# Performance work log

Measured on AMD Instinct MI355X. Metric: run time of the kernel, lower is better.

The kernel has to match this reference:

```python
import jax, jax.numpy as jnp
import numpy as np

B = 4096
HIST = 50
VOCAB = 100000
PAD_IDX = 179
EMB_DIM = 64           # sparse_dim_after_embedding
DENSE = 256            # dense_feature_number
PROJ_IN = 768          # emb_feature_dim_before_project
PROJ_HID = 256
PROJ_OUT = 64          # emb_feature_dim
BOT = (512, 64)        # bottom_mlp_dims
ALL_DIM = EMB_DIM + BOT[1] + PROJ_OUT        # 192
OUT_DIM = ALL_DIM * (ALL_DIM + 1) // 2 + BOT[1]  # 18592
TOP = (1024, 512)      # top_mlp_dims
BN_EPS = 1e-5

# precomputed upper-triangular (incl. diagonal) indices, row-major like torch mask extract
_TRIU_R, _TRIU_C = np.triu_indices(ALL_DIM)


def setup_inputs() -> dict:
    key = jax.random.key(0)
    ks = jax.random.split(key, 20)
    s = 0.02
    emb_table = jax.random.normal(ks[0], (VOCAB, EMB_DIM), jnp.float32) * s
    emb_table = emb_table.at[PAD_IDX].set(0.0)  # padding_idx=179
    return {
        "x_sparse": jax.random.randint(ks[1], (B, HIST), 0, VOCAB),
        "x_dense": jax.random.normal(ks[2], (B, DENSE), jnp.float32),
        "x_embed_before_projection": jax.random.normal(ks[3], (B, PROJ_IN), jnp.float32),
        "emb_table": emb_table,
        "pw1": jax.random.normal(ks[4], (PROJ_IN, PROJ_HID), jnp.float32) * s,
        "pb1": jnp.zeros((PROJ_HID,), jnp.float32),
        "pw2": jax.random.normal(ks[5], (PROJ_HID, PROJ_OUT), jnp.float32) * s,
        "pb2": jnp.zeros((PROJ_OUT,), jnp.float32),
        "bn_gamma": jnp.ones((PROJ_OUT,), jnp.float32),
        "bn_beta": jnp.zeros((PROJ_OUT,), jnp.float32),
        "bw1": jax.random.normal(ks[6], (DENSE, BOT[0]), jnp.float32) * s,
        "bb1": jnp.zeros((BOT[0],), jnp.float32),
        "bw2": jax.random.normal(ks[7], (BOT[0], BOT[1]), jnp.float32) * s,
        "bb2": jnp.zeros((BOT[1],), jnp.float32),
        "tw1": jax.random.normal(ks[8], (OUT_DIM, TOP[0]), jnp.float32) * s,
        "tb1": jnp.zeros((TOP[0],), jnp.float32),
        "tw2": jax.random.normal(ks[9], (TOP[0], TOP[1]), jnp.float32) * s,
        "tb2": jnp.zeros((TOP[1],), jnp.float32),
        "tw3": jax.random.normal(ks[10], (TOP[1], 1), jnp.float32) * s,
        "tb3": jnp.zeros((1,), jnp.float32),
    }


def reference(x_sparse, x_dense, x_embed_before_projection, emb_table,
              pw1, pb1, pw2, pb2, bn_gamma, bn_beta,
              bw1, bb1, bw2, bb2, tw1, tb1, tw2, tb2, tw3, tb3):
    # embedding-sum over history: [B, HIST, EMB_DIM] -> [B, EMB_DIM]
    embed_x = jnp.sum(emb_table[x_sparse], axis=1)

    # ContrastiveNet: Linear -> ReLU -> Linear -> BatchNorm1d (batch stats, training fwd)
    h = jax.nn.relu(x_embed_before_projection @ pw1 + pb1)
    z = h @ pw2 + pb2
    mu = jnp.mean(z, axis=0)
    var = jnp.var(z, axis=0)  # biased variance, as torch BN uses for normalization
    x_embed = bn_gamma * (z - mu) * jax.lax.rsqrt(var + BN_EPS) + bn_beta

    # bottom MLP (dropout = identity at inference)
    bottom = jax.nn.relu(jax.nn.relu(x_dense @ bw1 + bb1) @ bw2 + bb2)

    concat_first = jnp.concatenate([bottom, x_embed, embed_x], axis=-1)  # [B, 192]

    # pairwise dot-product interaction; pack upper triangle incl. diagonal
    dot = jnp.einsum('bi,bj->bij', concat_first, concat_first)  # [B, 192, 192]
    interaction = dot[:, _TRIU_R, _TRIU_C]  # [B, 192*193/2]

    concat_second = jnp.concatenate([interaction, bottom], axis=-1)  # [B, OUT_DIM]

    t = jax.nn.relu(concat_second @ tw1 + tb1)
    t = jax.nn.relu(t @ tw2 + tb2)
    output = jax.nn.sigmoid(t @ tw3 + tb3)  # [B, 1]
    # squeeze(-1).squeeze().unsqueeze(1) -> [B, 1]
    output = output.reshape(-1, 1)
    return output, x_embed
```

## Files before the change

kernel.cpp:

```cpp
#include <hip/hip_runtime.h>
#include <hip/hip_bf16.h>
#include <cstdint>
#include <cstddef>

typedef __bf16 bf16;
typedef unsigned char u8;
typedef __bf16 v8bf  __attribute__((ext_vector_type(8)));
typedef float  f32x4 __attribute__((ext_vector_type(4)));
typedef float  f32x16 __attribute__((ext_vector_type(16)));
typedef int    i32x4 __attribute__((ext_vector_type(4)));
typedef int    v8i32 __attribute__((ext_vector_type(8)));

__device__ __forceinline__ void async16(void* lds, const void* g) {
  __builtin_amdgcn_global_load_lds(
      (const __attribute__((address_space(1))) unsigned int*)g,
      (__attribute__((address_space(3))) unsigned int*)lds, 16, 0, 0);
}



__device__ __forceinline__ void pairs_dev(int* __restrict__ pairs) {
  int r = threadIdx.x;
  if (r < 192) {
    int off = 192 * r - (r * (r - 1)) / 2;
    for (int c = r; c < 192; ++c) pairs[off + c - r] = (r << 16) | c;
  } else if (r == 192) {
    for (int j = 0; j < 64; ++j) pairs[18528 + j] = (j << 16) | 192;
  } else if (r == 193) {
    for (int j = 18592; j < 18624; ++j) pairs[j] = (192 << 16) | 192;
  }
}

__device__ __forceinline__ void packA_dev(const float* __restrict__ A,
                                          bf16* __restrict__ Ap, int K,
                                          int bx, int by) {
  const int t = threadIdx.x;
  const int KT = K >> 5;
  const size_t tile = ((size_t)bx * KT + by) * (64 * 32);
  const int c = t;
  const int mm = c >> 2, koct = (c & 3) * 8;
  const float* src = A + (size_t)(bx * 64 + mm) * K + by * 32 + koct;
  f32x4 f0 = *(const f32x4*)src;
  f32x4 f1 = *(const f32x4*)(src + 4);
  __align__(16) bf16 h[8];
  h[0]=(bf16)f0[0]; h[1]=(bf16)f0[1]; h[2]=(bf16)f0[2]; h[3]=(bf16)f0[3];
  h[4]=(bf16)f1[0]; h[5]=(bf16)f1[1]; h[6]=(bf16)f1[2]; h[7]=(bf16)f1[3];
  *(i32x4*)(Ap + tile + (size_t)c * 8) = *(const i32x4*)h;
}

__device__ __forceinline__ void packB_dev(const float* __restrict__ B,
                                          bf16* __restrict__ Bp, int K, int N,
                                          int bx, int by,
                                          float* __restrict__ sLB) {
  const int BNp = 64, LS = 66;
  const int t = threadIdx.x;
  const int KT = K >> 5;
  for (int idx = t; idx < 32 * BNp; idx += 256) {
    const int kk = idx >> 6, nn = idx & 63;
    sLB[kk * LS + nn] = B[(size_t)(by * 32 + kk) * N + bx * BNp + nn];
  }
  __syncthreads();
  const size_t tile = ((size_t)bx * KT + by) * ((size_t)BNp * 32);
  for (int c = t; c < BNp * 4; c += 256) {
    const int nn = c >> 2, koct = (c & 3) * 8;
    __align__(16) bf16 h[8];
#pragma unroll
    for (int j = 0; j < 8; ++j) h[j] = (bf16)sLB[(koct + j) * LS + nn];
    *(i32x4*)(Bp + tile + (size_t)c * 8) = *(const i32x4*)h;
  }
}

__device__ __forceinline__ void packTw1_dev(const float* __restrict__ tw1,
                                            u8* __restrict__ Bp, int nt, int kw,
                                            float* __restrict__ sLB) {
  const int t = threadIdx.x;
  for (int idx = t; idx < 64 * 128; idx += 256) {
    const int kk = idx >> 7, nn = idx & 127;
    const int gk = kw * 64 + kk;
    sLB[kk * 130 + nn] = (gk < 18592) ? tw1[(size_t)gk * 1024 + nt * 128 + nn] * 32.f : 0.f;
  }
  __syncthreads();
  u8* tile = Bp + ((size_t)nt * 291 + kw) * 8192;
  for (int c = t; c < 512; c += 256) {
    const int nn = c >> 2, kb = (c & 3) * 16;
    i32x4 d;
#pragma unroll
    for (int g = 0; g < 4; ++g) {
      const float p0 = sLB[(kb + g * 4 + 0) * 130 + nn];
      const float p1 = sLB[(kb + g * 4 + 1) * 130 + nn];
      const float p2 = sLB[(kb + g * 4 + 2) * 130 + nn];
      const float p3 = sLB[(kb + g * 4 + 3) * 130 + nn];
      int r = __builtin_amdgcn_cvt_pk_fp8_f32(p0, p1, 0, false);
      r = __builtin_amdgcn_cvt_pk_fp8_f32(p2, p3, r, true);
      d[g] = r;
    }
    *(i32x4*)(tile + c * 16) = d;
  }
}

__device__ __forceinline__ void embed_dev(const int* __restrict__ xs,
                                          const float* __restrict__ emb,
                                          float* __restrict__ cf, int blk) {
  const int wid = threadIdx.x >> 6, lane = threadIdx.x & 63;
  const int b = blk * 4 + wid;
  const int* row = xs + (size_t)b * 50;
  float acc = 0.f;
  for (int h = 0; h < 50; ++h) {
    int idx = row[h];
    acc += emb[(size_t)idx * 64 + lane];
  }
  cf[(size_t)b * 193 + 128 + lane] = acc;
}

__global__ __launch_bounds__(256) void prologue_kernel(
    const float* __restrict__ xep, const float* __restrict__ xd,
    const float* __restrict__ pw1, const float* __restrict__ pw2,
    const float* __restrict__ bw1, const float* __restrict__ bw2,
    const float* __restrict__ tw1, const float* __restrict__ tw2,
    const int* __restrict__ xs, const float* __restrict__ emb,
    bf16* Xp, bf16* Xd, bf16* Bpw1, bf16* Bpw2, bf16* Bbw1, bf16* Bbw2,
    u8* Btw1, bf16* Btw2, float* cf, int* pairs) {
  __shared__ float sLB[64 * 130];
  int i = blockIdx.x;
  if (i < 2328) { packTw1_dev(tw1, Btw1, i & 7, i >> 3, sLB); return; }
  i -= 2328;
  if (i < 1536) { packA_dev(xep, Xp, 768, i & 63, i >> 6); return; }
  i -= 1536;
  if (i < 512)  { packA_dev(xd, Xd, 256, i & 63, i >> 6); return; }
  i -= 512;
  if (i < 96)   { packB_dev(pw1, Bpw1, 768, 256, i & 3, i >> 2, sLB); return; }
  i -= 96;
  if (i < 8)    { packB_dev(pw2, Bpw2, 256, 64, 0, i, sLB); return; }
  i -= 8;
  if (i < 64)   { packB_dev(bw1, Bbw1, 256, 512, i & 7, i >> 3, sLB); return; }
  i -= 64;
  if (i < 16)   { packB_dev(bw2, Bbw2, 512, 64, 0, i, sLB); return; }
  i -= 16;
  if (i < 256)  { packB_dev(tw2, Btw2, 1024, 512, i & 7, i >> 3, sLB); return; }
  i -= 256;
  if (i < 1024) { embed_dev(xs, emb, cf, i); return; }
  i -= 1024;
  if (i == 0) pairs_dev(pairs);
}

template <int BM, int BN, int MF, int NF>
__device__ __forceinline__ void gemm_body(
    const bf16* __restrict__ Ap, const bf16* __restrict__ Bp,
    const float* __restrict__ bias,
    float* __restrict__ outF, int ldF,
    bf16* __restrict__ outP, int ktN, int bmsh,
    int KT, int M0, int relu_flag, int bx, int by,
    bf16* sA, bf16* sB) {
  const int t = threadIdx.x;
  const int wid = t >> 6, lane = t & 63;
  const int wm = (wid >> 1) * (MF * 16);
  const int wn = (wid & 1) * (NF * 16);
  const int r16 = lane & 15, q = lane >> 4;

  f32x4 acc[MF][NF];
#pragma unroll
  for (int i = 0; i < MF; ++i)
#pragma unroll
    for (int j = 0; j < NF; ++j) acc[i][j] = f32x4{0.f, 0.f, 0.f, 0.f};

  const bf16* aBase = Ap + (size_t)bx * KT * (BM * 32);
  const bf16* bBase = Bp + (size_t)by * KT * (BN * 32);
  constexpr int A_CH = BM * 4;
  constexpr int B_CH = BN * 4;

  for (int kt = 0; kt < KT; ++kt) {
    const bf16* ag = aBase + (size_t)kt * (BM * 32);
    const bf16* bg = bBase + (size_t)kt * (BN * 32);
#pragma unroll
    for (int c = t; c < A_CH; c += 256) {
      const int row = c >> 2, qs = c & 3, qg = (qs - (row >> 1)) & 3;
      async16(sA + c * 8, ag + row * 32 + qg * 8);
    }
#pragma unroll
    for (int c = t; c < B_CH; c += 256) {
      const int row = c >> 2, qs = c & 3, qg = (qs - (row >> 1)) & 3;
      async16(sB + c * 8, bg + row * 32 + qg * 8);
    }
    __syncthreads();
    v8bf af[MF], bfr[NF];
#pragma unroll
    for (int i = 0; i < MF; ++i) {
      const int row = wm + i * 16 + r16;
      af[i] = *(const v8bf*)(sA + row * 32 + (((q + (row >> 1)) & 3) * 8));
    }
#pragma unroll
    for (int j = 0; j < NF; ++j) {
      const int row = wn + j * 16 + r16;
      bfr[j] = *(const v8bf*)(sB + row * 32 + (((q + (row >> 1)) & 3) * 8));
    }
#pragma unroll
    for (int i = 0; i < MF; ++i)
#pragma unroll
      for (int j = 0; j < NF; ++j)
        acc[i][j] = __builtin_amdgcn_mfma_f32_16x16x32_bf16(af[i], bfr[j], acc[i][j], 0, 0, 0);
    __syncthreads();
  }

#pragma unroll
  for (int j = 0; j < NF; ++j) {
    const int gn = by * BN + wn + j * 16 + r16;
    const float bv = bias[gn];
#pragma unroll
    for (int i = 0; i < MF; ++i) {
      const int gm0 = M0 + bx * BM + wm + i * 16 + q * 4;
#pragma unroll
      for (int r = 0; r < 4; ++r) {
        float v = acc[i][j][r] + bv;
        if (relu_flag) v = fmaxf(v, 0.f);
        const int gm = gm0 + r;
        if (outF) outF[(size_t)gm * ldF + gn] = v;
        if (outP) {
          const int mt = gm >> bmsh, mm = gm & ((1 << bmsh) - 1);
          outP[(((size_t)mt * ktN + (gn >> 5)) << (bmsh + 5)) + ((size_t)mm << 5) + (gn & 31)] = (bf16)v;
        }
      }
    }
  }
}

template <int BM, int BN, int MF, int NF>
__global__ __launch_bounds__(256, 2) void gemm_kernel(
    const bf16* __restrict__ Ap, const bf16* __restrict__ Bp,
    const float* __restrict__ bias,
    float* __restrict__ outF, int ldF,
    bf16* __restrict__ outP, int ktN, int bmsh,
    int KT, int M0, int relu_flag) {
  __shared__ __align__(16) bf16 sA[BM * 32];
  __shared__ __align__(16) bf16 sB[BN * 32];
  gemm_body<BM, BN, MF, NF>(Ap, Bp, bias, outF, ldF, outP, ktN, bmsh,
                            KT, M0, relu_flag, blockIdx.x, blockIdx.y, sA, sB);
}

template <int BM, int BN, int MF, int NF>
__global__ __launch_bounds__(256, 2) void gemm_dual_kernel(
    const bf16* Ap0, const bf16* Bp0, const float* bias0,
    float* outF0, int ldF0, bf16* outP0, int ktN0, int bmsh0, int KT0, int relu0, int gy0,
    const bf16* Ap1, const bf16* Bp1, const float* bias1,
    float* outF1, int ldF1, bf16* outP1, int ktN1, int bmsh1, int KT1, int relu1, int gy1) {
  __shared__ __align__(16) bf16 sA[BM * 32];
  __shared__ __align__(16) bf16 sB[BN * 32];
  if (blockIdx.z == 0) {
    if ((int)blockIdx.y >= gy0) return;
    gemm_body<BM, BN, MF, NF>(Ap0, Bp0, bias0, outF0, ldF0, outP0, ktN0, bmsh0,
                              KT0, 0, relu0, blockIdx.x, blockIdx.y, sA, sB);
  } else {
    if ((int)blockIdx.y >= gy1) return;
    gemm_body<BM, BN, MF, NF>(Ap1, Bp1, bias1, outF1, ldF1, outP1, ktN1, bmsh1,
                              KT1, 0, relu1, blockIdx.x, blockIdx.y, sA, sB);
  }
}

__global__ __launch_bounds__(256, 2) void gemm_splitk_mx(
    const u8* __restrict__ Ap, const u8* __restrict__ Bp,
    bf16* __restrict__ part, int S, int Mchunk) {
  __shared__ __align__(16) u8 sA[2][8192];
  __shared__ __align__(16) u8 sB[2][8192];
  const int t = threadIdx.x;
  const int bx = blockIdx.x, by = blockIdx.y, bz = blockIdx.z;
  const int wid = t >> 6, lane = t & 63;
  const int wm = (wid >> 1) * 64, wn = (wid & 1) * 64;
  const int l31 = lane & 31, khalf = lane >> 5;
  const int kw0 = (291 * bz) / S, kw1 = (291 * (bz + 1)) / S;

  f32x16 acc[2][2];
#pragma unroll
  for (int i = 0; i < 2; ++i)
#pragma unroll
    for (int j = 0; j < 2; ++j)
#pragma unroll
      for (int r = 0; r < 16; ++r) acc[i][j][r] = 0.f;

  const u8* aBase = Ap + (size_t)bx * 291 * 8192;
  const u8* bBase = Bp + (size_t)by * 291 * 8192;

  auto stage = [&](int buf, int kw) {
    const u8* ag = aBase + (size_t)kw * 8192;
    const u8* bg = bBase + (size_t)kw * 8192;
#pragma unroll
    for (int c = t; c < 512; c += 256) {
      const int row = c >> 2, qs = c & 3, qg = (qs - (row >> 1)) & 3;
      async16(sA[buf] + c * 16, ag + row * 64 + qg * 16);
    }
#pragma unroll
    for (int c = t; c < 512; c += 256) {
      const int row = c >> 2, qs = c & 3, qg = (qs - (row >> 1)) & 3;
      async16(sB[buf] + c * 16, bg + row * 64 + qg * 16);
    }
  };
  auto frag = [&](const u8* s, int row) -> v8i32 {
    const int q0 = (khalf * 2 + (row >> 1)) & 3;
    const int q1 = (khalf * 2 + 1 + (row >> 1)) & 3;
    union { i32x4 h[2]; v8i32 v; } u;
    u.h[0] = *(const i32x4*)(s + row * 64 + q0 * 16);
    u.h[1] = *(const i32x4*)(s + row * 64 + q1 * 16);
    return u.v;
  };
  auto compute = [&](int buf) {
    v8i32 av[2], bv[2];
#pragma unroll
    for (int i = 0; i < 2; ++i) av[i] = frag(sA[buf], wm + i * 32 + l31);
#pragma unroll
    for (int j = 0; j < 2; ++j) bv[j] = frag(sB[buf], wn + j * 32 + l31);
#pragma unroll
    for (int i = 0; i < 2; ++i)
#pragma unroll
      for (int j = 0; j < 2; ++j)
        acc[i][j] = __builtin_amdgcn_mfma_scale_f32_32x32x64_f8f6f4(
            av[i], bv[j], acc[i][j], 0, 0,
            0, 0x7F7F7F7F,
            0, 0x7A7A7A7A);
  };

  int kw = kw0;
  for (; kw + 1 < kw1; kw += 2) {
    stage(0, kw);
    stage(1, kw + 1);
    __syncthreads();
    compute(0);
    compute(1);
    __syncthreads();
  }
  if (kw < kw1) {
    stage(0, kw);
    __syncthreads();
    compute(0);
    __syncthreads();
  }

  bf16* pBase = part + (size_t)bz * Mchunk * 1024;
#pragma unroll
  for (int i = 0; i < 2; ++i)
#pragma unroll
    for (int j = 0; j < 2; ++j) {
      const int gn = by * 128 + wn + j * 32 + l31;
#pragma unroll
      for (int r = 0; r < 16; ++r) {
        const int gm = bx * 128 + wm + i * 32 + (r & 3) + 8 * (r >> 2) + 4 * khalf;
        pBase[(size_t)gm * 1024 + gn] = (bf16)acc[i][j][r];
      }
    }
}

__global__ __launch_bounds__(256) void reducek_kernel(const bf16* __restrict__ part,
                                                      const float* __restrict__ bias,
                                                      bf16* __restrict__ t1,
                                                      int S, int Mchunk, int M0) {
  const int idx = blockIdx.x * 256 + threadIdx.x;
  const int gm = idx >> 7;
  const int gn8 = (idx & 127) * 8;
  float v[8] = {0.f, 0.f, 0.f, 0.f, 0.f, 0.f, 0.f, 0.f};
  for (int s = 0; s < S; ++s) {
    v8bf p = *(const v8bf*)(part + ((size_t)s * Mchunk + gm) * 1024 + gn8);
#pragma unroll
    for (int r = 0; r < 8; ++r) v[r] += (float)p[r];
  }
  const f32x4 b0 = *(const f32x4*)(bias + gn8);
  const f32x4 b1 = *(const f32x4*)(bias + gn8 + 4);
  __align__(16) bf16 h[8];
#pragma unroll
  for (int r = 0; r < 4; ++r) h[r] = (bf16)fmaxf(v[r] + b0[r], 0.f);
#pragma unroll
  for (int r = 0; r < 4; ++r) h[4 + r] = (bf16)fmaxf(v[4 + r] + b1[r], 0.f);
  const int G = M0 + gm;
  const int mt = G >> 6, mm = G & 63, kt = gn8 >> 5;
  *(i32x4*)(t1 + (((size_t)mt * 32 + kt) << 11) + (mm << 5) + (gn8 & 31)) = *(const i32x4*)h;
}

__global__ __launch_bounds__(256) void bnstats_kernel(const float* __restrict__ z,
                                                      float* __restrict__ stats) {
  const int j = blockIdx.x, t = threadIdx.x;
  float s = 0.f, s2 = 0.f;
  for (int b = t; b < 4096; b += 256) {
    float v = z[(size_t)b * 64 + j];
    s += v; s2 += v * v;
  }
  __shared__ float sh[256], sh2[256];
  sh[t] = s; sh2[t] = s2;
  __syncthreads();
  for (int o = 128; o > 0; o >>= 1) {
    if (t < o) { sh[t] += sh[t + o]; sh2[t] += sh2[t + o]; }
    __syncthreads();
  }
  if (t == 0) {
    float mu = sh[0] * (1.f / 4096.f);
    float var = sh2[0] * (1.f / 4096.f) - mu * mu;
    stats[j] = mu;
    stats[64 + j] = rsqrtf(var + 1e-5f);
  }
}

__global__ __launch_bounds__(256) void cfbuild_kernel(const float* __restrict__ z,
                                                      const float* __restrict__ stats,
                                                      const float* __restrict__ gamma,
                                                      const float* __restrict__ beta,
                                                      float* __restrict__ cf,
                                                      float* __restrict__ dout) {
  const int wid = threadIdx.x >> 6, lane = threadIdx.x & 63;
  const int b = blockIdx.x * 4 + wid;
  const float mu = stats[lane], rstd = stats[64 + lane];
  const float xe = gamma[lane] * (z[(size_t)b * 64 + lane] - mu) * rstd + beta[lane];
  cf[(size_t)b * 193 + 64 + lane] = xe;
  dout[4096 + (size_t)b * 64 + lane] = xe;
  if (lane == 0) cf[(size_t)b * 193 + 192] = 1.f;
}

__global__ __launch_bounds__(256, 2) void agen_kernel(const float* __restrict__ cf,
                                                      const int* __restrict__ pairs,
                                                      u8* __restrict__ Ap, int rowBase) {
  __shared__ float sCF[64 * 193];
  const int t = threadIdx.x;
  const int gRow0 = rowBase + blockIdx.x * 64;
  for (int i = t; i < 64 * 193; i += 256) sCF[i] = cf[(size_t)gRow0 * 193 + i];
  __syncthreads();
  const int kw0 = (291 * blockIdx.y) / 8;
  const int kw1 = (291 * (blockIdx.y + 1)) / 8;
  const int row = t >> 2, kq = t & 3;
  const int mt = blockIdx.x >> 1;
  const int mrow = (blockIdx.x & 1) * 64 + row;
  const float* myrow = sCF + row * 193;
  for (int kw = kw0; kw < kw1; ++kw) {
    const int kb = kw * 64 + kq * 16;
    i32x4 d;
#pragma unroll
    for (int g = 0; g < 4; ++g) {
      float p[4];
#pragma unroll
      for (int j = 0; j < 4; ++j) {
        const int pr = pairs[kb + g * 4 + j];
        p[j] = myrow[pr >> 16] * myrow[pr & 0xffff];
      }
      int r = __builtin_amdgcn_cvt_pk_fp8_f32(p[0], p[1], 0, false);
      r = __builtin_amdgcn_cvt_pk_fp8_f32(p[2], p[3], r, true);
      d[g] = r;
    }
    *(i32x4*)(Ap + (((size_t)mt * 291 + kw) * 128 + mrow) * 64 + kq * 16) = d;
  }
}

__global__ __launch_bounds__(256) void topdot_kernel(const float* __restrict__ t2,
                                                     const float* __restrict__ w,
                                                     const float* __restrict__ b3,
                                                     float* __restrict__ dout) {
  const int wid = threadIdx.x >> 6, lane = threadIdx.x & 63;
  const int b = blockIdx.x * 4 + wid;
  const f32x4* row = (const f32x4*)(t2 + (size_t)b * 512);
  const f32x4* wv = (const f32x4*)w;
  float s = 0.f;
#pragma unroll
  for (int i = 0; i < 2; ++i) {
    f32x4 a = row[lane * 2 + i], c = wv[lane * 2 + i];
    s += a[0] * c[0] + a[1] * c[1] + a[2] * c[2] + a[3] * c[3];
  }
  for (int m = 32; m > 0; m >>= 1) s += __shfl_xor(s, m, 64);
  if (lane == 0) dout[b] = 1.f / (1.f + __expf(-(s + b3[0])));
}

extern "C" void kernel_launch(void* const* d_in, const int* in_sizes, int n_in,
                              void* d_out, int out_size, void* d_ws, size_t ws_size,
                              hipStream_t stream) {
  const int*   xs   = (const int*)  d_in[0];
  const float* xd   = (const float*)d_in[1];
  const float* xep  = (const float*)d_in[2];
  const float* emb  = (const float*)d_in[3];
  const float* pw1  = (const float*)d_in[4];
  const float* pb1  = (const float*)d_in[5];
  const float* pw2  = (const float*)d_in[6];
  const float* pb2  = (const float*)d_in[7];
  const float* gmma = (const float*)d_in[8];
  const float* beta = (const float*)d_in[9];
  const float* bw1  = (const float*)d_in[10];
  const float* bb1  = (const float*)d_in[11];
  const float* bw2  = (const float*)d_in[12];
  const float* bb2  = (const float*)d_in[13];
  const float* tw1  = (const float*)d_in[14];
  const float* tb1  = (const float*)d_in[15];
  const float* tw2  = (const float*)d_in[16];
  const float* tb2  = (const float*)d_in[17];
  const float* tw3  = (const float*)d_in[18];
  const float* tb3  = (const float*)d_in[19];
  float* out = (float*)d_out;

  uint8_t* base = (uint8_t*)d_ws;
  size_t off = 0;
  auto alloc = [&](size_t b) {
    void* p = base + off;
    off = (off + b + 511) & ~((size_t)511);
    return p;
  };
  int*  pairs = (int*) alloc((size_t)18624 * 4);
  bf16* Xp    = (bf16*)alloc((size_t)4096 * 768 * 2);
  bf16* Xd    = (bf16*)alloc((size_t)4096 * 256 * 2);
  bf16* Bpw1  = (bf16*)alloc((size_t)768 * 256 * 2);
  bf16* Bpw2  = (bf16*)alloc((size_t)256 * 64 * 2);
  bf16* Bbw1  = (bf16*)alloc((size_t)256 * 512 * 2);
  bf16* Bbw2  = (bf16*)alloc((size_t)512 * 64 * 2);
  u8*   Btw1  = (u8*)  alloc((size_t)8 * 291 * 8192);
  bf16* Btw2  = (bf16*)alloc((size_t)1024 * 512 * 2);
  bf16* hbuf  = (bf16*)alloc((size_t)4096 * 256 * 2);
  float* z    = (float*)alloc((size_t)4096 * 64 * 4);
  float* stats= (float*)alloc((size_t)128 * 4);
  bf16* b0    = (bf16*)alloc((size_t)4096 * 512 * 2);
  float* cf   = (float*)alloc((size_t)4096 * 193 * 4);
  bf16* t1    = (bf16*)alloc((size_t)4096 * 1024 * 2);
  float* t2   = (float*)alloc((size_t)4096 * 512 * 4);
  size_t fixedEnd = off;

  int chunk = 512, S = 8;
  {
    const int candC[5] = {4096, 4096, 2048, 1024, 512};
    const int candS[5] = {8, 4, 8, 8, 8};
    for (int i = 0; i < 5; ++i) {
      size_t need = fixedEnd + (size_t)candC[i] * 18624 + 1024 +
                    (size_t)candS[i] * candC[i] * 1024 * 2 + 1024;
      if (need <= ws_size) { chunk = candC[i]; S = candS[i]; break; }
    }
  }
  u8*   ApBig = (u8*)  alloc((size_t)chunk * 18624);
  bf16* partK = (bf16*)alloc((size_t)S * chunk * 1024 * 2);

  prologue_kernel<<<5841, 256, 0, stream>>>(
      xep, xd, pw1, pw2, bw1, bw2, tw1, tw2, xs, emb,
      Xp, Xd, Bpw1, Bpw2, Bbw1, Bbw2, Btw1, Btw2, cf, pairs);

  gemm_dual_kernel<64, 64, 2, 2><<<dim3(64, 8, 2), 256, 0, stream>>>(
      Xp, Bpw1, pb1, nullptr, 0, hbuf, 8, 6, 24, 1, 4,
      Xd, Bbw1, bb1, nullptr, 0, b0, 16, 6, 8, 1, 8);
  gemm_dual_kernel<64, 64, 2, 2><<<dim3(64, 1, 2), 256, 0, stream>>>(
      hbuf, Bpw2, pb2, z, 64, nullptr, 0, 0, 8, 0, 1,
      b0, Bbw2, bb2, cf, 193, nullptr, 0, 0, 16, 1, 1);

  bnstats_kernel<<<64, 256, 0, stream>>>(z, stats);
  cfbuild_kernel<<<1024, 256, 0, stream>>>(z, stats, gmma, beta, cf, out);

  for (int c0 = 0; c0 < 4096; c0 += chunk) {
    agen_kernel<<<dim3(chunk / 64, 8), 256, 0, stream>>>(cf, pairs, ApBig, c0);
    gemm_splitk_mx<<<dim3(chunk / 128, 8, S), 256, 0, stream>>>(
        ApBig, Btw1, partK, S, chunk);
    reducek_kernel<<<chunk / 2, 256, 0, stream>>>(partK, tb1, t1, S, chunk, c0);
  }

  gemm_kernel<64, 64, 2, 2><<<dim3(64, 8), 256, 0, stream>>>(
      t1, Btw2, tb2, t2, 512, nullptr, 0, 0, 32, 0, 1);
  topdot_kernel<<<1024, 256, 0, stream>>>(t2, tw3, tb3, out);
}
```

Before: 383.0 us.

## Vectorize tw1 packing, shrink pair table, move embedding into dual GEMM

Several changes land together. The tw1 fp8 packing now uses float4 loads into a smaller two-phase LDS tile (32x132). The pair index table is compressed to 16-bit entries that are loaded as vectors in agen. The embedding-bag sum moves out of the prologue into a third z-slice of the first dual GEMM launch, with 8 rows per block, so it overlaps with the GEMMs. The occupancy hint on the split-K fp8 GEMM is also raised to 3 blocks per SM, which may increase register pressure.

```diff
diff --git a/kernel.cpp b/kernel.cpp
--- a/kernel.cpp
+++ b/kernel.cpp
@@ -5,6 +5,7 @@
 
 typedef __bf16 bf16;
 typedef unsigned char u8;
+typedef unsigned short u16;
 typedef __bf16 v8bf  __attribute__((ext_vector_type(8)));
 typedef float  f32x4 __attribute__((ext_vector_type(4)));
 typedef float  f32x16 __attribute__((ext_vector_type(16)));
@@ -19,15 +20,15 @@
 
 
 
-__device__ __forceinline__ void pairs_dev(int* __restrict__ pairs) {
+__device__ __forceinline__ void pairs_dev(u16* __restrict__ pairs) {
   int r = threadIdx.x;
   if (r < 192) {
     int off = 192 * r - (r * (r - 1)) / 2;
-    for (int c = r; c < 192; ++c) pairs[off + c - r] = (r << 16) | c;
+    for (int c = r; c < 192; ++c) pairs[off + c - r] = (u16)((r << 8) | c);
   } else if (r == 192) {
-    for (int j = 0; j < 64; ++j) pairs[18528 + j] = (j << 16) | 192;
+    for (int j = 0; j < 64; ++j) pairs[18528 + j] = (u16)((j << 8) | 192);
   } else if (r == 193) {
-    for (int j = 18592; j < 18624; ++j) pairs[j] = (192 << 16) | 192;
+    for (int j = 18592; j < 18624; ++j) pairs[j] = (u16)((192 << 8) | 192);
   }
 }
 
@@ -74,42 +75,38 @@
                                             u8* __restrict__ Bp, int nt, int kw,
                                             float* __restrict__ sLB) {
   const int t = threadIdx.x;
-  for (int idx = t; idx < 64 * 128; idx += 256) {
-    const int kk = idx >> 7, nn = idx & 127;
-    const int gk = kw * 64 + kk;
-    sLB[kk * 130 + nn] = (gk < 18592) ? tw1[(size_t)gk * 1024 + nt * 128 + nn] * 32.f : 0.f;
-  }
-  __syncthreads();
   u8* tile = Bp + ((size_t)nt * 291 + kw) * 8192;
-  for (int c = t; c < 512; c += 256) {
-    const int nn = c >> 2, kb = (c & 3) * 16;
+#pragma unroll
+  for (int ph = 0; ph < 2; ++ph) {
+    if (ph) __syncthreads();
+#pragma unroll
+    for (int idx = t; idx < 1024; idx += 256) {
+      const int kk = idx >> 5, nn4 = (idx & 31) * 4;
+      const int gk = kw * 64 + ph * 32 + kk;
+      f32x4 v = f32x4{0.f, 0.f, 0.f, 0.f};
+      if (gk < 18592) {
+        v = *(const f32x4*)(tw1 + (size_t)gk * 1024 + nt * 128 + nn4);
+        v *= 32.f;
+      }
+      *(f32x4*)(sLB + kk * 132 + nn4) = v;
+    }
+    __syncthreads();
+    const int nn = t >> 1;
+    const int hkb = (t & 1) * 16;
+    const int c = nn * 4 + ph * 2 + (t & 1);
     i32x4 d;
 #pragma unroll
     for (int g = 0; g < 4; ++g) {
-      const float p0 = sLB[(kb + g * 4 + 0) * 130 + nn];
-      const float p1 = sLB[(kb + g * 4 + 1) * 130 + nn];
-      const float p2 = sLB[(kb + g * 4 + 2) * 130 + nn];
-      const float p3 = sLB[(kb + g * 4 + 3) * 130 + nn];
+      const float p0 = sLB[(hkb + g * 4 + 0) * 132 + nn];
+      const float p1 = sLB[(hkb + g * 4 + 1) * 132 + nn];
+      const float p2 = sLB[(hkb + g * 4 + 2) * 132 + nn];
+      const float p3 = sLB[(hkb + g * 4 + 3) * 132 + nn];
       int r = __builtin_amdgcn_cvt_pk_fp8_f32(p0, p1, 0, false);
       r = __builtin_amdgcn_cvt_pk_fp8_f32(p2, p3, r, true);
       d[g] = r;
     }
     *(i32x4*)(tile + c * 16) = d;
   }
-}
-
-__device__ __forceinline__ void embed_dev(const int* __restrict__ xs,
-                                          const float* __restrict__ emb,
-                                          float* __restrict__ cf, int blk) {
-  const int wid = threadIdx.x >> 6, lane = threadIdx.x & 63;
-  const int b = blk * 4 + wid;
-  const int* row = xs + (size_t)b * 50;
-  float acc = 0.f;
-  for (int h = 0; h < 50; ++h) {
-    int idx = row[h];
-    acc += emb[(size_t)idx * 64 + lane];
-  }
-  cf[(size_t)b * 193 + 128 + lane] = acc;
 }
 
 __global__ __launch_bounds__(256) void prologue_kernel(
@@ -117,10 +114,9 @@
     const float* __restrict__ pw1, const float* __restrict__ pw2,
     const float* __restrict__ bw1, const float* __restrict__ bw2,
     const float* __restrict__ tw1, const float* __restrict__ tw2,
-    const int* __restrict__ xs, const float* __restrict__ emb,
     bf16* Xp, bf16* Xd, bf16* Bpw1, bf16* Bpw2, bf16* Bbw1, bf16* Bbw2,
-    u8* Btw1, bf16* Btw2, float* cf, int* pairs) {
-  __shared__ float sLB[64 * 130];
+    u8* Btw1, bf16* Btw2, u16* pairs) {
+  __shared__ float sLB[32 * 132];
   int i = blockIdx.x;
   if (i < 2328) { packTw1_dev(tw1, Btw1, i & 7, i >> 3, sLB); return; }
   i -= 2328;
@@ -138,9 +134,24 @@
   i -= 16;
   if (i < 256)  { packB_dev(tw2, Btw2, 1024, 512, i & 7, i >> 3, sLB); return; }
   i -= 256;
-  if (i < 1024) { embed_dev(xs, emb, cf, i); return; }
-  i -= 1024;
   if (i == 0) pairs_dev(pairs);
+}
+
+__device__ __forceinline__ void embed8_dev(const int* __restrict__ xs,
+                                           const float* __restrict__ emb,
+                                           float* __restrict__ cf, int blk) {
+  const int wid = threadIdx.x >> 6, lane = threadIdx.x & 63;
+#pragma unroll
+  for (int s = 0; s < 2; ++s) {
+    const int b = blk * 8 + s * 4 + wid;
+    const int* row = xs + (size_t)b * 50;
+    float acc = 0.f;
+    for (int h = 0; h < 50; ++h) {
+      int idx = row[h];
+      acc += emb[(size_t)idx * 64 + lane];
+    }
+    cf[(size_t)b * 193 + 128 + lane] = acc;
+  }
 }
 
 template <int BM, int BN, int MF, int NF>
@@ -241,21 +252,24 @@
     const bf16* Ap0, const bf16* Bp0, const float* bias0,
     float* outF0, int ldF0, bf16* outP0, int ktN0, int bmsh0, int KT0, int relu0, int gy0,
     const bf16* Ap1, const bf16* Bp1, const float* bias1,
-    float* outF1, int ldF1, bf16* outP1, int ktN1, int bmsh1, int KT1, int relu1, int gy1) {
+    float* outF1, int ldF1, bf16* outP1, int ktN1, int bmsh1, int KT1, int relu1, int gy1,
+    const int* xs, const float* emb, float* cf) {
   __shared__ __align__(16) bf16 sA[BM * 32];
   __shared__ __align__(16) bf16 sB[BN * 32];
   if (blockIdx.z == 0) {
     if ((int)blockIdx.y >= gy0) return;
     gemm_body<BM, BN, MF, NF>(Ap0, Bp0, bias0, outF0, ldF0, outP0, ktN0, bmsh0,
                               KT0, 0, relu0, blockIdx.x, blockIdx.y, sA, sB);
-  } else {
+  } else if (blockIdx.z == 1) {
     if ((int)blockIdx.y >= gy1) return;
     gemm_body<BM, BN, MF, NF>(Ap1, Bp1, bias1, outF1, ldF1, outP1, ktN1, bmsh1,
                               KT1, 0, relu1, blockIdx.x, blockIdx.y, sA, sB);
-  }
-}
-
-__global__ __launch_bounds__(256, 2) void gemm_splitk_mx(
+  } else {
+    embed8_dev(xs, emb, cf, blockIdx.y * 64 + blockIdx.x);
+  }
+}
+
+__global__ __launch_bounds__(256, 3) void gemm_splitk_mx(
     const u8* __restrict__ Ap, const u8* __restrict__ Bp,
     bf16* __restrict__ part, int S, int Mchunk) {
   __shared__ __align__(16) u8 sA[2][8192];
@@ -410,7 +424,7 @@
 }
 
 __global__ __launch_bounds__(256, 2) void agen_kernel(const float* __restrict__ cf,
-                                                      const int* __restrict__ pairs,
+                                                      const u16* __restrict__ pairs,
                                                       u8* __restrict__ Ap, int rowBase) {
   __shared__ float sCF[64 * 193];
   const int t = threadIdx.x;
@@ -425,14 +439,17 @@
   const float* myrow = sCF + row * 193;
   for (int kw = kw0; kw < kw1; ++kw) {
     const int kb = kw * 64 + kq * 16;
+    union { i32x4 v4[2]; u16 u[16]; } P;
+    P.v4[0] = *(const i32x4*)(pairs + kb);
+    P.v4[1] = *(const i32x4*)(pairs + kb + 8);
     i32x4 d;
 #pragma unroll
     for (int g = 0; g < 4; ++g) {
       float p[4];
 #pragma unroll
       for (int j = 0; j < 4; ++j) {
-        const int pr = pairs[kb + g * 4 + j];
-        p[j] = myrow[pr >> 16] * myrow[pr & 0xffff];
+        const u16 pr = P.u[g * 4 + j];
+        p[j] = myrow[pr >> 8] * myrow[pr & 255];
       }
       int r = __builtin_amdgcn_cvt_pk_fp8_f32(p[0], p[1], 0, false);
       r = __builtin_amdgcn_cvt_pk_fp8_f32(p[2], p[3], r, true);
@@ -492,7 +509,7 @@
     off = (off + b + 511) & ~((size_t)511);
     return p;
   };
-  int*  pairs = (int*) alloc((size_t)18624 * 4);
+  u16*  pairs = (u16*) alloc((size_t)18624 * 2);
   bf16* Xp    = (bf16*)alloc((size_t)4096 * 768 * 2);
   bf16* Xd    = (bf16*)alloc((size_t)4096 * 256 * 2);
   bf16* Bpw1  = (bf16*)alloc((size_t)768 * 256 * 2);
@@ -523,16 +540,18 @@
   u8*   ApBig = (u8*)  alloc((size_t)chunk * 18624);
   bf16* partK = (bf16*)alloc((size_t)S * chunk * 1024 * 2);
 
-  prologue_kernel<<<5841, 256, 0, stream>>>(
-      xep, xd, pw1, pw2, bw1, bw2, tw1, tw2, xs, emb,
-      Xp, Xd, Bpw1, Bpw2, Bbw1, Bbw2, Btw1, Btw2, cf, pairs);
-
-  gemm_dual_kernel<64, 64, 2, 2><<<dim3(64, 8, 2), 256, 0, stream>>>(
+  prologue_kernel<<<4817, 256, 0, stream>>>(
+      xep, xd, pw1, pw2, bw1, bw2, tw1, tw2,
+      Xp, Xd, Bpw1, Bpw2, Bbw1, Bbw2, Btw1, Btw2, pairs);
+
+  gemm_dual_kernel<64, 64, 2, 2><<<dim3(64, 8, 3), 256, 0, stream>>>(
       Xp, Bpw1, pb1, nullptr, 0, hbuf, 8, 6, 24, 1, 4,
-      Xd, Bbw1, bb1, nullptr, 0, b0, 16, 6, 8, 1, 8);
+      Xd, Bbw1, bb1, nullptr, 0, b0, 16, 6, 8, 1, 8,
+      xs, emb, cf);
   gemm_dual_kernel<64, 64, 2, 2><<<dim3(64, 1, 2), 256, 0, stream>>>(
       hbuf, Bpw2, pb2, z, 64, nullptr, 0, 0, 8, 0, 1,
-      b0, Bbw2, bb2, cf, 193, nullptr, 0, 0, 16, 1, 1);
+      b0, Bbw2, bb2, cf, 193, nullptr, 0, 0, 16, 1, 1,
+      nullptr, nullptr, nullptr);
 
   bnstats_kernel<<<64, 256, 0, stream>>>(z, stats);
   cfbuild_kernel<<<1024, 256, 0, stream>>>(z, stats, gmma, beta, cf, out);
```

After: 360.6 us. 1.06x faster.
